# Optimization experiments

Measured on AMD Instinct MI355X. Metric: run time of the kernel, lower is better.

Reference implementation:

```python
import jax, jax.numpy as jnp
import numpy as np

EPS = 1e-6

def _ln(x, g, b):
    m = jnp.mean(x, -1, keepdims=True)
    v = jnp.mean((x - m) ** 2, -1, keepdims=True)
    return (x - m) * jax.lax.rsqrt(v + 1e-5) * g + b

def _mha(qin, kin, vin, wq, bq, wk, bk, wv, bv, wo, bo, nh=8):
    B, T, D = qin.shape
    S = kin.shape[1]
    dh = D // nh
    q = (qin @ wq + bq).reshape(B, T, nh, dh)
    k = (kin @ wk + bk).reshape(B, S, nh, dh)
    v = (vin @ wv + bv).reshape(B, S, nh, dh)
    a = jax.nn.softmax(jnp.einsum('bthd,bshd->bhts', q, k) / np.float32(np.sqrt(dh)), -1)
    o = jnp.einsum('bhts,bshd->bthd', a, v).reshape(B, T, D)
    return o @ wo + bo

def _sinu_pe(pos, num_feats=128, temperature=20.0):
    # pos: [..., 2] (x, y); returns [..., 2*num_feats] ordered (y-feats, x-feats)
    dim_t = temperature ** ((2 * (jnp.arange(num_feats) // 2)) / num_feats)
    e = pos[..., None] * (2 * np.pi) / dim_t  # [..., 2, F]
    e = jnp.stack([jnp.sin(e[..., 0::2]), jnp.cos(e[..., 1::2])], -1).reshape(e.shape)
    return jnp.concatenate([e[..., 1, :], e[..., 0, :]], -1)

def _spatial36(b1, b2, sizes):
    # b1, b2: [B, Q, 4]; sizes: [B, 2] = (h, w). UPT-style 18 feats + log -> 36.
    h = sizes[:, 0:1]; w = sizes[:, 1:2]
    c1x = (b1[..., 0] + b1[..., 2]) / 2; c1y = (b1[..., 1] + b1[..., 3]) / 2
    c2x = (b2[..., 0] + b2[..., 2]) / 2; c2y = (b2[..., 1] + b2[..., 3]) / 2
    w1 = b1[..., 2] - b1[..., 0]; h1 = b1[..., 3] - b1[..., 1]
    w2 = b2[..., 2] - b2[..., 0]; h2 = b2[..., 3] - b2[..., 1]
    a1 = w1 * h1; a2 = w2 * h2
    dx = jnp.abs(c2x - c1x) / (w1 + EPS)
    dy = jnp.abs(c2y - c1y) / (h1 + EPS)
    ix = jnp.clip(jnp.minimum(b1[..., 2], b2[..., 2]) - jnp.maximum(b1[..., 0], b2[..., 0]), 0)
    iy = jnp.clip(jnp.minimum(b1[..., 3], b2[..., 3]) - jnp.maximum(b1[..., 1], b2[..., 1]), 0)
    inter = ix * iy
    iou = inter / (a1 + a2 - inter + EPS)
    f = jnp.stack([c1x / w, c1y / h, c2x / w, c2y / h, w1 / w, h1 / h, w2 / w, h2 / h,
                   a1 / (h * w), a2 / (h * w), a2 / (a1 + EPS), w1 / (h1 + EPS), w2 / (h2 + EPS), iou,
                   (c2x > c1x) * dx, (c2x < c1x) * dx, (c2y > c1y) * dy, (c2y < c1y) * dy], -1)
    return jnp.concatenate([f, jnp.log(f + EPS)], -1)

def _forward(boxes, embeds, image_sizes, pose, line, sw1, sb1, sw2, sb2, sw3, sb3, bw, bb, pw, pb, lw, lb, enc_pe_w, enc_pe_b, enc_qkv_w, enc_qkv_b, enc_out_w, enc_out_b, enc_ff1_w, enc_ff1_b, enc_ff2_w, enc_ff2_b, enc_ln1_g, enc_ln1_b, enc_ln2_g, enc_ln2_b, dec_q_w, dec_q_b, dec_kv_w, dec_kv_b, dec_out_w, dec_out_b, dec_ff1_w, dec_ff1_b, dec_ff2_w, dec_ff2_b, dec_ln1_g, dec_ln1_b, dec_ln2_g, dec_ln2_b, fc1_w, fc1_b, fc2_w, fc2_b, mln1_g, mln1_b, mln2_g, mln2_b, m1_w, m1_b, m2_w, m2_b, labels, nh):
    B, N, _ = boxes.shape
    # static human-object pairing (x != y) & (x < nh)
    xg, yg = np.meshgrid(np.arange(N), np.arange(N), indexing='ij')
    keep = (xg != yg) & (xg < nh)
    xk = jnp.asarray(xg[keep]); yk = jnp.asarray(yg[keep])  # [P]
    # line features: adaptive-avg-pool(1,1) + 1x1 conv == spatial mean + linear
    line_feat = jnp.mean(line, axis=(2, 3)) @ lw + lb  # [B, 256]
    # spatial head on all N*N ordered pairs, then gather kept pairs
    xa = jnp.asarray(xg.reshape(-1)); ya = jnp.asarray(yg.reshape(-1))
    f36 = _spatial36(boxes[:, xa], boxes[:, ya], image_sizes)  # [B, N*N, 36]
    s = jax.nn.relu(f36 @ sw1 + sb1)
    s = jax.nn.relu(s @ sw2 + sb2)
    s = jax.nn.relu(s @ sw3 + sb3)
    spa = s.reshape(B, N, N, -1)[:, xk, yk]  # [B, P, R]
    # box sinusoidal positional encodings (cat of centre-PE and wh-PE)
    whwh = image_sizes[:, jnp.array([1, 0, 1, 0])][:, None]  # [B,1,4]
    bxn = boxes / whwh
    ctr = (bxn[..., :2] + bxn[..., 2:]) / 2
    whb = bxn[..., 2:] - bxn[..., :2]
    box_pe = jnp.concatenate([_sinu_pe(ctr), _sinu_pe(whb)], -1)  # [B, N, 512]
    # 2-layer transformer encoder over instance tokens (pos added to q,k)
    posx = box_pe @ enc_pe_w + enc_pe_b
    x = embeds
    for i in range(enc_qkv_w.shape[0]):
        wq, wk_, wv = jnp.split(enc_qkv_w[i], 3, axis=1)
        bq, bk_, bv = jnp.split(enc_qkv_b[i], 3)
        qk = x + posx
        att = _mha(qk, qk, x, wq, bq, wk_, bk_, wv, bv, enc_out_w[i], enc_out_b[i])
        x = _ln(x + att, enc_ln1_g[i], enc_ln1_b[i])
        ff = jax.nn.relu(x @ enc_ff1_w[i] + enc_ff1_b[i]) @ enc_ff2_w[i] + enc_ff2_b[i]
        x = _ln(x + ff, enc_ln2_g[i], enc_ln2_b[i])
    # pair gather + human/object positional embeds (box PE projected + line feature)
    pe_h = box_pe[:, xk] @ bw + bb + line_feat[:, None, :]
    pe_o = box_pe[:, yk] @ bw + bb + line_feat[:, None, :]
    h = x[:, xk]; o = x[:, yk]  # [B, P, 256]
    pose_ctx = pose @ pw + pb  # [B, M, 256]
    # HO refine decoder: cross-attention from pair tokens to pose tokens
    for l in range(dec_q_w.shape[0]):
        wk_, wv = jnp.split(dec_kv_w[l], 2, axis=1)
        bk_, bv = jnp.split(dec_kv_b[l], 2)
        def _layer(feat, pe):
            att = _mha(feat + pe, pose_ctx, pose_ctx, dec_q_w[l], dec_q_b[l], wk_, bk_, wv, bv, dec_out_w[l], dec_out_b[l])
            feat = _ln(feat + att, dec_ln1_g[l], dec_ln1_b[l])
            ff = jax.nn.relu(feat @ dec_ff1_w[l] + dec_ff1_b[l]) @ dec_ff2_w[l] + dec_ff2_b[l]
            return _ln(feat + ff, dec_ln2_g[l], dec_ln2_b[l])
        h = _layer(h, pe_h)
        o = _layer(o, pe_o)
    # multi-modal fusion
    ho = jnp.concatenate([h, o], -1)  # [B, P, 512]
    ho = _ln(ho @ fc1_w + fc1_b, mln1_g, mln1_b)
    sp = _ln(spa @ fc2_w + fc2_b, mln2_g, mln2_b)
    z = jax.nn.relu(jnp.concatenate([ho, sp], -1))
    z = jax.nn.relu(z @ m1_w + m1_b)
    z = jax.nn.relu(z @ m2_w + m2_b)
    return z  # [B, P, 256] HOI query features

def setup_inputs() -> dict:
    key = jax.random.key(0)
    ks = iter(jax.random.split(key, 80))
    B, N, NH, M, HH, WW = 16, 128, 32, 64, 8, 8
    W = 0.05
    def rn(shape, s=1.0):
        return jax.random.normal(next(ks), shape, dtype=jnp.float32) * s
    def ru(shape):
        return jax.random.uniform(next(ks), shape, dtype=jnp.float32)
    sizes = 800.0 + 480.0 * ru((B, 2))  # (h, w)
    wh = sizes[:, jnp.array([1, 0])]
    xy = ru((B, N, 2)) * wh[:, None] * 0.7
    bwh = ru((B, N, 2)) * wh[:, None] * 0.25 + 4.0
    boxes = jnp.concatenate([xy, xy + bwh], -1)
    labels = jnp.concatenate([jnp.zeros((B, NH), jnp.int32), jax.random.randint(next(ks), (B, N - NH), 1, 81, dtype=jnp.int32)], -1)
    return dict(
        boxes=boxes, embeds=rn((B, N, 256)), image_sizes=sizes, pose=rn((B, M, 768)), line=rn((B, 2048, HH, WW)),
        sw1=rn((36, 128), W), sb1=jnp.zeros((128,)), sw2=rn((128, 256), W), sb2=jnp.zeros((256,)), sw3=rn((256, 256), W), sb3=jnp.zeros((256,)),
        bw=rn((512, 256), W), bb=jnp.zeros((256,)), pw=rn((768, 256), W), pb=jnp.zeros((256,)), lw=rn((2048, 256), W), lb=jnp.zeros((256,)),
        enc_pe_w=rn((512, 256), W), enc_pe_b=jnp.zeros((256,)),
        enc_qkv_w=rn((2, 256, 768), W), enc_qkv_b=jnp.zeros((2, 768)), enc_out_w=rn((2, 256, 256), W), enc_out_b=jnp.zeros((2, 256)),
        enc_ff1_w=rn((2, 256, 1024), W), enc_ff1_b=jnp.zeros((2, 1024)), enc_ff2_w=rn((2, 1024, 256), W), enc_ff2_b=jnp.zeros((2, 256)),
        enc_ln1_g=jnp.ones((2, 256)), enc_ln1_b=jnp.zeros((2, 256)), enc_ln2_g=jnp.ones((2, 256)), enc_ln2_b=jnp.zeros((2, 256)),
        dec_q_w=rn((2, 256, 256), W), dec_q_b=jnp.zeros((2, 256)), dec_kv_w=rn((2, 256, 512), W), dec_kv_b=jnp.zeros((2, 512)),
        dec_out_w=rn((2, 256, 256), W), dec_out_b=jnp.zeros((2, 256)),
        dec_ff1_w=rn((2, 256, 1024), W), dec_ff1_b=jnp.zeros((2, 1024)), dec_ff2_w=rn((2, 1024, 256), W), dec_ff2_b=jnp.zeros((2, 256)),
        dec_ln1_g=jnp.ones((2, 256)), dec_ln1_b=jnp.zeros((2, 256)), dec_ln2_g=jnp.ones((2, 256)), dec_ln2_b=jnp.zeros((2, 256)),
        fc1_w=rn((512, 256), W), fc1_b=jnp.zeros((256,)), fc2_w=rn((256, 256), W), fc2_b=jnp.zeros((256,)),
        mln1_g=jnp.ones((256,)), mln1_b=jnp.zeros((256,)), mln2_g=jnp.ones((256,)), mln2_b=jnp.zeros((256,)),
        m1_w=rn((512, 384), W), m1_b=jnp.zeros((384,)), m2_w=rn((384, 256), W), m2_b=jnp.zeros((256,)),
        labels=labels, nh=NH)

def reference(boxes, embeds, image_sizes, pose, line, sw1, sb1, sw2, sb2, sw3, sb3, bw, bb, pw, pb, lw, lb, enc_pe_w, enc_pe_b, enc_qkv_w, enc_qkv_b, enc_out_w, enc_out_b, enc_ff1_w, enc_ff1_b, enc_ff2_w, enc_ff2_b, enc_ln1_g, enc_ln1_b, enc_ln2_g, enc_ln2_b, dec_q_w, dec_q_b, dec_kv_w, dec_kv_b, dec_out_w, dec_out_b, dec_ff1_w, dec_ff1_b, dec_ff2_w, dec_ff2_b, dec_ln1_g, dec_ln1_b, dec_ln2_g, dec_ln2_b, fc1_w, fc1_b, fc2_w, fc2_b, mln1_g, mln1_b, mln2_g, mln2_b, m1_w, m1_b, m2_w, m2_b, labels, nh):
    return _forward(boxes, embeds, image_sizes, pose, line, sw1, sb1, sw2, sb2, sw3, sb3, bw, bb, pw, pb, lw, lb, enc_pe_w, enc_pe_b, enc_qkv_w, enc_qkv_b, enc_out_w, enc_out_b, enc_ff1_w, enc_ff1_b, enc_ff2_w, enc_ff2_b, enc_ln1_g, enc_ln1_b, enc_ln2_g, enc_ln2_b, dec_q_w, dec_q_b, dec_kv_w, dec_kv_b, dec_out_w, dec_out_b, dec_ff1_w, dec_ff1_b, dec_ff2_w, dec_ff2_b, dec_ln1_g, dec_ln1_b, dec_ln2_g, dec_ln2_b, fc1_w, fc1_b, fc2_w, fc2_b, mln1_g, mln1_b, mln2_g, mln2_b, m1_w, m1_b, m2_w, m2_b, labels, nh)
```

## Files before the change

### kernel.cpp

```cpp
#include <hip/hip_runtime.h>
#include <stdint.h>

static constexpr int B      = 16;
static constexpr int N      = 128;
static constexpr int P      = 4064;
static constexpr int MPOSE  = 64;
static constexpr int64_t BN = (int64_t)B * N;
static constexpr int64_t BP = (int64_t)B * P;

#define TWO_PI 6.283185307179586f
#define QSCALE 0.17677669529663687f

typedef __attribute__((ext_vector_type(4))) float f32x4;
typedef __attribute__((ext_vector_type(8))) short bf16x8;
typedef __attribute__((ext_vector_type(8))) unsigned short u16x8;
typedef __attribute__((ext_vector_type(4))) unsigned short u16x4;

__device__ __forceinline__ unsigned short f2bf(float f) {
    union { float f; unsigned u; } v; v.f = f;
    unsigned r = (v.u + 0x7fffu + ((v.u >> 16) & 1u)) >> 16;
    return (unsigned short)r;
}
__device__ __forceinline__ float bf2f(unsigned short u) {
    union { unsigned u; float f; } v; v.u = (unsigned)u << 16;
    return v.f;
}
__device__ __forceinline__ void pair_xy(int p, int& x, int& y) {
    x = p / 127;
    int r = p - x * 127;
    y = (r < x) ? r : r + 1;
}
__device__ __forceinline__ int xcd_swz(int orig, int nwg) {
    int q = nwg >> 3, r = nwg & 7;
    int xcd = orig & 7, idx = orig >> 3;
    return (xcd < r ? xcd * (q + 1) : r * (q + 1) + (xcd - r) * q) + idx;
}
__device__ __forceinline__ void gld16(const unsigned short* g, unsigned short* l) {
    __builtin_amdgcn_global_load_lds(
        (const __attribute__((address_space(1))) void*)g,
        (__attribute__((address_space(3))) void*)l, 16, 0, 0);
}

struct WDesc { const float* src; int64_t dstOff; int K, Nn, Kpad, blockStart; };
struct WTable { WDesc d[29]; int nDesc; };

__global__ __launch_bounds__(256) void wprep_all_k(WTable t, unsigned short* __restrict__ wt)
{
    __shared__ float s[32][33];
    int bid = blockIdx.x;
    int di = 0;
    for (int i = 1; i < t.nDesc; ++i) if (t.d[i].blockStart <= bid) di = i;
    const WDesc& d = t.d[di];
    int lbid = bid - d.blockStart;
    int kTiles = d.Kpad >> 5;
    int k0 = (lbid % kTiles) * 32, n0 = (lbid / kTiles) * 32;
    int tx = threadIdx.x & 31, ty = threadIdx.x >> 5;
#pragma unroll
    for (int i = 0; i < 4; ++i) {
        int k = k0 + ty + i * 8;
        s[ty + i * 8][tx] = (k < d.K) ? d.src[(int64_t)k * d.Nn + n0 + tx] : 0.f;
    }
    __syncthreads();
    unsigned short* dst = wt + d.dstOff;
#pragma unroll
    for (int i = 0; i < 4; ++i) {
        int n = n0 + ty + i * 8;
        dst[(int64_t)n * d.Kpad + k0 + tx] = f2bf(s[tx][ty + i * 8]);
    }
}

template <bool RELU_OUT>
__global__ __launch_bounds__(256) void bgemm_k(
    const float* __restrict__ A, const float* __restrict__ A2, int lda,
    const unsigned short* __restrict__ Bt, int ldk,
    const float* __restrict__ bias,
    const float* __restrict__ Cadd, int addLd,
    const float* __restrict__ lfp,
    float* __restrict__ C, int ldc,
    int kSteps)
{
    __shared__ unsigned short As[128][40];
    __shared__ unsigned short Bs[128][40];
    const int tid  = threadIdx.x;
    const int lane = tid & 63;
    const int wave = tid >> 6;
    const int wr = wave >> 1, wc = wave & 1;
    const int row0 = blockIdx.y * 128, col0 = blockIdx.x * 128;
    const int l15 = lane & 15, l4 = lane >> 4;
    const int sr = tid >> 1;
    const int sh = (tid & 1) * 16;

    f32x4 acc[4][4] = {};

    for (int ks = 0; ks < kSteps; ++ks) {
        const int k0 = ks * 32;
        {
            const int64_t off = (int64_t)(row0 + sr) * lda + k0 + sh;
            const float* ap = A + off;
            float v[16];
#pragma unroll
            for (int i = 0; i < 4; ++i) {
                float4 tv = ((const float4*)ap)[i];
                v[i*4+0] = tv.x; v[i*4+1] = tv.y; v[i*4+2] = tv.z; v[i*4+3] = tv.w;
            }
            if (A2) {
                const float* ap2 = A2 + off;
#pragma unroll
                for (int i = 0; i < 4; ++i) {
                    float4 tv = ((const float4*)ap2)[i];
                    v[i*4+0] += tv.x; v[i*4+1] += tv.y; v[i*4+2] += tv.z; v[i*4+3] += tv.w;
                }
            }
            u16x8 p0, p1;
#pragma unroll
            for (int j = 0; j < 8; ++j) { p0[j] = f2bf(v[j]); p1[j] = f2bf(v[8 + j]); }
            *(u16x8*)&As[sr][sh]     = p0;
            *(u16x8*)&As[sr][sh + 8] = p1;
        }
        {
            const unsigned short* bp = Bt + (int64_t)(col0 + sr) * ldk + k0 + sh;
            *(u16x8*)&Bs[sr][sh]     = *(const u16x8*)bp;
            *(u16x8*)&Bs[sr][sh + 8] = *(const u16x8*)(bp + 8);
        }
        __syncthreads();
        bf16x8 af[4], bfr[4];
#pragma unroll
        for (int f = 0; f < 4; ++f) {
            af[f]  = *(const bf16x8*)&As[wr * 64 + f * 16 + l15][l4 * 8];
            bfr[f] = *(const bf16x8*)&Bs[wc * 64 + f * 16 + l15][l4 * 8];
        }
#pragma unroll
        for (int i = 0; i < 4; ++i)
#pragma unroll
            for (int j = 0; j < 4; ++j)
                acc[i][j] = __builtin_amdgcn_mfma_f32_16x16x32_bf16(af[i], bfr[j], acc[i][j], 0, 0, 0);
        __syncthreads();
    }
#pragma unroll
    for (int i = 0; i < 4; ++i) {
        int rb = row0 + wr * 64 + i * 16 + l4 * 4;
#pragma unroll
        for (int j = 0; j < 4; ++j) {
            int c = col0 + wc * 64 + j * 16 + l15;
            float bv = bias ? bias[c] : 0.f;
#pragma unroll
            for (int e = 0; e < 4; ++e) {
                int r = rb + e;
                float vv = acc[i][j][e] + bv;
                if (Cadd && c < addLd) vv += Cadd[(int64_t)r * addLd + c];
                if (lfp) vv += lfp[(r >> 7) * 256 + c];
                if (RELU_OUT) vv = fmaxf(vv, 0.f);
                C[(int64_t)r * ldc + c] = vv;
            }
        }
    }
}

static void bgemm(hipStream_t st,
                  const float* A, const float* A2, int lda,
                  const unsigned short* Bt, int ldk, const float* bias,
                  const float* Cadd, int addLd, const float* lfp,
                  float* C, int ldc, int M, int Ncols, int K, bool reluOut)
{
    dim3 g(Ncols / 128, M / 128), b(256);
    if (reluOut) bgemm_k<true><<<g,b,0,st>>>(A,A2,lda,Bt,ldk,bias,Cadd,addLd,lfp,C,ldc,K/32);
    else         bgemm_k<false><<<g,b,0,st>>>(A,A2,lda,Bt,ldk,bias,Cadd,addLd,lfp,C,ldc,K/32);
}

__global__ __launch_bounds__(256) void tgemm_k(
    const float* __restrict__ A, int lda,
    const unsigned short* __restrict__ Bt, int ldk,
    const float* __restrict__ bias,
    const float* __restrict__ res,
    const float* __restrict__ g, const float* __restrict__ be,
    float* __restrict__ C, int kSteps)
{
    __shared__ unsigned short As[64][40];
    __shared__ unsigned short Bs[256][40];
    __shared__ float partS[64][4], partQ[64][4];
    __shared__ float statM[64], statI[64];
    const int tid = threadIdx.x;
    const int lane = tid & 63, w = tid >> 6;
    const int l15 = lane & 15, l4 = lane >> 4;
    const int row0 = blockIdx.x * 64;
    const int sra = tid >> 2, sha = (tid & 3) * 8;

    f32x4 acc[4][4] = {};
    for (int ks = 0; ks < kSteps; ++ks) {
        int k0 = ks * 32;
        {
            const float* ap = A + (int64_t)(row0 + sra) * lda + k0 + sha;
            float4 t0 = ((const float4*)ap)[0];
            float4 t1 = ((const float4*)ap)[1];
            u16x8 p;
            p[0]=f2bf(t0.x); p[1]=f2bf(t0.y); p[2]=f2bf(t0.z); p[3]=f2bf(t0.w);
            p[4]=f2bf(t1.x); p[5]=f2bf(t1.y); p[6]=f2bf(t1.z); p[7]=f2bf(t1.w);
            *(u16x8*)&As[sra][sha] = p;
        }
        {
            const unsigned short* bp = Bt + (int64_t)tid * ldk + k0;
#pragma unroll
            for (int q = 0; q < 4; ++q)
                *(u16x8*)&Bs[tid][q * 8] = *(const u16x8*)(bp + q * 8);
        }
        __syncthreads();
        bf16x8 af[4], bfr[4];
#pragma unroll
        for (int f = 0; f < 4; ++f) {
            af[f]  = *(const bf16x8*)&As[f * 16 + l15][l4 * 8];
            bfr[f] = *(const bf16x8*)&Bs[w * 64 + f * 16 + l15][l4 * 8];
        }
#pragma unroll
        for (int i = 0; i < 4; ++i)
#pragma unroll
            for (int j = 0; j < 4; ++j)
                acc[i][j] = __builtin_amdgcn_mfma_f32_16x16x32_bf16(af[i], bfr[j], acc[i][j], 0, 0, 0);
        __syncthreads();
    }
    float ps[4][4] = {}, pq[4][4] = {};
#pragma unroll
    for (int i = 0; i < 4; ++i)
#pragma unroll
    for (int j = 0; j < 4; ++j) {
        int c = w * 64 + j * 16 + l15;
#pragma unroll
        for (int e = 0; e < 4; ++e) {
            int r = i * 16 + l4 * 4 + e;
            float v = acc[i][j][e] + bias[c] + res[(int64_t)(row0 + r) * 256 + c];
            acc[i][j][e] = v;
            ps[i][e] += v;
            pq[i][e] += v * v;
        }
    }
#pragma unroll
    for (int i = 0; i < 4; ++i)
#pragma unroll
    for (int e = 0; e < 4; ++e) {
#pragma unroll
        for (int m = 1; m < 16; m <<= 1) {
            ps[i][e] += __shfl_xor(ps[i][e], m);
            pq[i][e] += __shfl_xor(pq[i][e], m);
        }
    }
    if (l15 == 0) {
#pragma unroll
        for (int i = 0; i < 4; ++i)
#pragma unroll
        for (int e = 0; e < 4; ++e) {
            int r = i * 16 + l4 * 4 + e;
            partS[r][w] = ps[i][e];
            partQ[r][w] = pq[i][e];
        }
    }
    __syncthreads();
    if (tid < 64) {
        float s = partS[tid][0] + partS[tid][1] + partS[tid][2] + partS[tid][3];
        float q = partQ[tid][0] + partQ[tid][1] + partQ[tid][2] + partQ[tid][3];
        float m = s * (1.f/256.f);
        float var = q * (1.f/256.f) - m * m;
        statM[tid] = m;
        statI[tid] = rsqrtf(var + 1e-5f);
    }
    __syncthreads();
#pragma unroll
    for (int i = 0; i < 4; ++i)
#pragma unroll
    for (int j = 0; j < 4; ++j) {
        int c = w * 64 + j * 16 + l15;
#pragma unroll
        for (int e = 0; e < 4; ++e) {
            int r = i * 16 + l4 * 4 + e;
            C[(int64_t)(row0 + r) * 256 + c] = (acc[i][j][e] - statM[r]) * statI[r] * g[c] + be[c];
        }
    }
}

template <bool RELU_OUT, bool OUT_BF16>
__global__ __launch_bounds__(256) void hgemm_k(
    const unsigned short* __restrict__ A, int lda,
    const unsigned short* __restrict__ Bt, int ldk,
    const float* __restrict__ bias,
    void* __restrict__ Cv, int ldc,
    int kSteps, int nx)
{
    __shared__ unsigned short As[128][32];
    __shared__ unsigned short Bs[128][32];
    const int tid  = threadIdx.x;
    const int lane = tid & 63;
    const int wave = tid >> 6;
    const int wr = wave >> 1, wc = wave & 1;
    const int wgid = xcd_swz(blockIdx.x, gridDim.x);
    const int row0 = (wgid / nx) * 128, col0 = (wgid % nx) * 128;
    const int l15 = lane & 15, l4 = lane >> 4;
    const int srow = lane >> 2;
    const int scol = (lane & 3) * 8;

    f32x4 acc[4][4] = {};

    for (int ks = 0; ks < kSteps; ++ks) {
        const int k0 = ks * 32;
#pragma unroll
        for (int i = 0; i < 2; ++i) {
            int seg = wave * 2 + i;
            int r = seg * 16 + srow;
            gld16(A  + (int64_t)(row0 + r) * lda + k0 + scol, &As[seg * 16][0]);
            gld16(Bt + (int64_t)(col0 + r) * ldk + k0 + scol, &Bs[seg * 16][0]);
        }
        __syncthreads();
        bf16x8 af[4], bfr[4];
#pragma unroll
        for (int f = 0; f < 4; ++f) {
            af[f]  = *(const bf16x8*)&As[wr * 64 + f * 16 + l15][l4 * 8];
            bfr[f] = *(const bf16x8*)&Bs[wc * 64 + f * 16 + l15][l4 * 8];
        }
#pragma unroll
        for (int i = 0; i < 4; ++i)
#pragma unroll
            for (int j = 0; j < 4; ++j)
                acc[i][j] = __builtin_amdgcn_mfma_f32_16x16x32_bf16(af[i], bfr[j], acc[i][j], 0, 0, 0);
        __syncthreads();
    }
#pragma unroll
    for (int i = 0; i < 4; ++i) {
        int rb = row0 + wr * 64 + i * 16 + l4 * 4;
#pragma unroll
        for (int j = 0; j < 4; ++j) {
            int c = col0 + wc * 64 + j * 16 + l15;
            float bv = bias ? bias[c] : 0.f;
#pragma unroll
            for (int e = 0; e < 4; ++e) {
                int64_t off = (int64_t)(rb + e) * ldc + c;
                float vv = acc[i][j][e] + bv;
                if (RELU_OUT) vv = fmaxf(vv, 0.f);
                if (OUT_BF16) ((unsigned short*)Cv)[off] = f2bf(vv);
                else          ((float*)Cv)[off] = vv;
            }
        }
    }
}

__global__ __launch_bounds__(256) void spa_k(
    const float* __restrict__ boxes, const float* __restrict__ sizes,
    const unsigned short* __restrict__ W1, const float* __restrict__ b1,
    const unsigned short* __restrict__ W2, const float* __restrict__ b2,
    unsigned short* __restrict__ t3out, int chunk0)
{
    __shared__ unsigned short F[128][72];
    __shared__ unsigned short Bs[128][40];
    __shared__ unsigned short D1s[128][136];
    const int tid  = threadIdx.x;
    const int lane = tid & 63;
    const int wave = tid >> 6;
    const int wr = wave >> 1, wc = wave & 1;
    const int row0 = blockIdx.x * 128;
    const int l15 = lane & 15, l4 = lane >> 4;
    const int sr = tid >> 1;
    const int sh = (tid & 1) * 16;

    if (tid < 128) {
        int gp = chunk0 + row0 + tid;
        int b = gp / P, p = gp - b * P;
        int xi, yi; pair_xy(p, xi, yi);
        const float* b1x = boxes + ((int64_t)b * N + xi) * 4;
        const float* b2x = boxes + ((int64_t)b * N + yi) * 4;
        float h = sizes[b * 2 + 0], w = sizes[b * 2 + 1];
        float c1x = (b1x[0] + b1x[2]) * 0.5f, c1y = (b1x[1] + b1x[3]) * 0.5f;
        float c2x = (b2x[0] + b2x[2]) * 0.5f, c2y = (b2x[1] + b2x[3]) * 0.5f;
        float w1 = b1x[2] - b1x[0], h1 = b1x[3] - b1x[1];
        float w2 = b2x[2] - b2x[0], h2 = b2x[3] - b2x[1];
        float a1 = w1 * h1, a2 = w2 * h2;
        float dx = fabsf(c2x - c1x) / (w1 + 1e-6f);
        float dy = fabsf(c2y - c1y) / (h1 + 1e-6f);
        float ix = fmaxf(fminf(b1x[2], b2x[2]) - fmaxf(b1x[0], b2x[0]), 0.f);
        float iy = fmaxf(fminf(b1x[3], b2x[3]) - fmaxf(b1x[1], b2x[1]), 0.f);
        float inter = ix * iy;
        float iou = inter / (a1 + a2 - inter + 1e-6f);
        float f[18];
        f[0] = c1x / w;  f[1] = c1y / h;  f[2] = c2x / w;  f[3] = c2y / h;
        f[4] = w1 / w;   f[5] = h1 / h;   f[6] = w2 / w;   f[7] = h2 / h;
        f[8] = a1 / (h * w); f[9] = a2 / (h * w); f[10] = a2 / (a1 + 1e-6f);
        f[11] = w1 / (h1 + 1e-6f); f[12] = w2 / (h2 + 1e-6f); f[13] = iou;
        f[14] = (c2x > c1x) ? dx : 0.f;  f[15] = (c2x < c1x) ? dx : 0.f;
        f[16] = (c2y > c1y) ? dy : 0.f;  f[17] = (c2y < c1y) ? dy : 0.f;
#pragma unroll
        for (int i = 0; i < 18; ++i) {
            F[tid][i]      = f2bf(f[i]);
            F[tid][18 + i] = f2bf(logf(f[i] + 1e-6f));
        }
#pragma unroll
        for (int i = 36; i < 64; ++i) F[tid][i] = 0;
    }
    __syncthreads();

    f32x4 acc1[4][4] = {};
    for (int ks = 0; ks < 2; ++ks) {
        const int k0 = ks * 32;
        {
            const unsigned short* bp = W1 + (int64_t)sr * 64 + k0 + sh;
            *(u16x8*)&Bs[sr][sh]     = *(const u16x8*)bp;
            *(u16x8*)&Bs[sr][sh + 8] = *(const u16x8*)(bp + 8);
        }
        __syncthreads();
        bf16x8 af[4], bfr[4];
#pragma unroll
        for (int f = 0; f < 4; ++f) {
            af[f]  = *(const bf16x8*)&F[wr * 64 + f * 16 + l15][k0 + l4 * 8];
            bfr[f] = *(const bf16x8*)&Bs[wc * 64 + f * 16 + l15][l4 * 8];
        }
#pragma unroll
        for (int i = 0; i < 4; ++i)
#pragma unroll
            for (int j = 0; j < 4; ++j)
                acc1[i][j] = __builtin_amdgcn_mfma_f32_16x16x32_bf16(af[i], bfr[j], acc1[i][j], 0, 0, 0);
        __syncthreads();
    }
#pragma unroll
    for (int i = 0; i < 4; ++i) {
        int rb = wr * 64 + i * 16 + l4 * 4;
#pragma unroll
        for (int j = 0; j < 4; ++j) {
            int c = wc * 64 + j * 16 + l15;
            float bv = b1[c];
#pragma unroll
            for (int e = 0; e < 4; ++e)
                D1s[rb + e][c] = f2bf(fmaxf(acc1[i][j][e] + bv, 0.f));
        }
    }
    __syncthreads();

    f32x4 acc2[2][4][4] = {};
#pragma unroll
    for (int n = 0; n < 2; ++n) {
        for (int kk = 0; kk < 4; ++kk) {
            {
                const unsigned short* bp = W2 + (int64_t)(n * 128 + sr) * 128 + kk * 32 + sh;
                *(u16x8*)&Bs[sr][sh]     = *(const u16x8*)bp;
                *(u16x8*)&Bs[sr][sh + 8] = *(const u16x8*)(bp + 8);
            }
            __syncthreads();
            bf16x8 af[4], bfr[4];
#pragma unroll
            for (int f = 0; f < 4; ++f) {
                af[f]  = *(const bf16x8*)&D1s[wr * 64 + f * 16 + l15][kk * 32 + l4 * 8];
                bfr[f] = *(const bf16x8*)&Bs[wc * 64 + f * 16 + l15][l4 * 8];
            }
#pragma unroll
            for (int i = 0; i < 4; ++i)
#pragma unroll
                for (int j = 0; j < 4; ++j)
                    acc2[n][i][j] = __builtin_amdgcn_mfma_f32_16x16x32_bf16(af[i], bfr[j], acc2[n][i][j], 0, 0, 0);
            __syncthreads();
// ... 29 lines not shown
    int b = gp / P, p = gp - b * P;
    int xi, yi; pair_xy(p, xi, yi);
    int c = lane * 4;
    {
        float4 u  = *(const float4*)(UV + ((int64_t)(b * 128 + xi)) * 512 + c);
        float4 vv = *(const float4*)(UV + ((int64_t)(b * 128 + yi)) * 512 + 256 + c);
        float4 fbv = *(const float4*)(fb + c);
        float4 v;
        v.x = u.x + vv.x + fbv.x; v.y = u.y + vv.y + fbv.y;
        v.z = u.z + vv.z + fbv.z; v.w = u.w + vv.w + fbv.w;
        float s  = v.x + v.y + v.z + v.w;
        float sq = v.x*v.x + v.y*v.y + v.z*v.z + v.w*v.w;
#pragma unroll
        for (int off = 1; off < 64; off <<= 1) {
            s  += __shfl_xor(s, off);
            sq += __shfl_xor(sq, off);
        }
        float m = s * (1.f/256.f);
        float var = sq * (1.f/256.f) - m * m;
        float inv = rsqrtf(var + 1e-5f);
        float4 gg = *(const float4*)(g1 + c);
        float4 bb = *(const float4*)(be1 + c);
        u16x4 o;
        o[0] = f2bf(fmaxf((v.x - m) * inv * gg.x + bb.x, 0.f));
        o[1] = f2bf(fmaxf((v.y - m) * inv * gg.y + bb.y, 0.f));
        o[2] = f2bf(fmaxf((v.z - m) * inv * gg.z + bb.z, 0.f));
        o[3] = f2bf(fmaxf((v.w - m) * inv * gg.w + bb.w, 0.f));
        *(u16x4*)(zb + (int64_t)li * 512 + c) = o;
    }
    {
        u16x4 u = *(const u16x4*)(t3 + (int64_t)li * 256 + c);
        float4 v;
        v.x = bf2f(u[0]); v.y = bf2f(u[1]); v.z = bf2f(u[2]); v.w = bf2f(u[3]);
        float s  = v.x + v.y + v.z + v.w;
        float sq = v.x*v.x + v.y*v.y + v.z*v.z + v.w*v.w;
#pragma unroll
        for (int off = 1; off < 64; off <<= 1) {
            s  += __shfl_xor(s, off);
            sq += __shfl_xor(sq, off);
        }
        float m = s * (1.f/256.f);
        float var = sq * (1.f/256.f) - m * m;
        float inv = rsqrtf(var + 1e-5f);
        float4 gg = *(const float4*)(g2 + c);
        float4 bb = *(const float4*)(be2 + c);
        u16x4 o;
        o[0] = f2bf(fmaxf((v.x - m) * inv * gg.x + bb.x, 0.f));
        o[1] = f2bf(fmaxf((v.y - m) * inv * gg.y + bb.y, 0.f));
        o[2] = f2bf(fmaxf((v.z - m) * inv * gg.z + bb.z, 0.f));
        o[3] = f2bf(fmaxf((v.w - m) * inv * gg.w + bb.w, 0.f));
        *(u16x4*)(zb + (int64_t)li * 512 + 256 + c) = o;
    }
}

__global__ __launch_bounds__(256) void line_mean_k(const float* __restrict__ line, float* __restrict__ lm)
{
    int wave = threadIdx.x >> 6, lane = threadIdx.x & 63;
    int bc = blockIdx.x * 4 + wave;
    float v = line[(int64_t)bc * 64 + lane];
#pragma unroll
    for (int off = 1; off < 64; off <<= 1) v += __shfl_xor(v, off);
    if (lane == 0) lm[bc] = v * (1.f/64.f);
}

__global__ __launch_bounds__(256) void line_proj_k(
    const float* __restrict__ lm, const float* __restrict__ lw,
    const float* __restrict__ lb, float* __restrict__ lf)
{
    __shared__ float red[8][32];
    int b = blockIdx.y, jg = blockIdx.x;
    int jj = threadIdx.x & 31, cc = threadIdx.x >> 5;
    int j = jg * 32 + jj;
    const float* lmb = lm + (int64_t)b * 2048 + cc * 256;
    const float* lwp = lw + (int64_t)(cc * 256) * 256 + j;
    float acc = 0.f;
#pragma unroll 4
    for (int k = 0; k < 256; ++k) acc += lmb[k] * lwp[(int64_t)k * 256];
    red[cc][jj] = acc;
    __syncthreads();
    if (cc == 0) {
        float s = lb[j];
#pragma unroll
        for (int i = 0; i < 8; ++i) s += red[i][jj];
        lf[b * 256 + j] = s;
    }
}

__global__ __launch_bounds__(512) void boxpe_k(
    const float* __restrict__ boxes, const float* __restrict__ sizes, float* __restrict__ boxpe)
{
    int row = blockIdx.x;
    int b = row >> 7;
    int i = threadIdx.x;
    const float* bx = boxes + (int64_t)row * 4;
    float h = sizes[b * 2 + 0], w = sizes[b * 2 + 1];
    float x0 = bx[0] / w, y0 = bx[1] / h, x1 = bx[2] / w, y1 = bx[3] / h;
    int seg = i >> 7, j = i & 127, k = j >> 1;
    float val;
    switch (seg) {
        case 0: val = (y0 + y1) * 0.5f; break;
        case 1: val = (x0 + x1) * 0.5f; break;
        case 2: val = (y1 - y0); break;
        default: val = (x1 - x0); break;
    }
    float dimt = exp2f((float)k * (4.321928094887362f / 64.f));
    float arg = val * TWO_PI / dimt;
    boxpe[(int64_t)row * 512 + i] = (j & 1) ? cosf(arg) : sinf(arg);
}

__global__ __launch_bounds__(128) void enc_attn_k(
    const float* __restrict__ qkv, float* __restrict__ outp)
{
    int b = blockIdx.x >> 3, hd = blockIdx.x & 7;
    __shared__ float kl[128][32];
    __shared__ float vl[128][32];
    int tid = threadIdx.x;
    for (int i = tid; i < 128 * 32; i += 128) {
        int s = i >> 5, j = i & 31;
        const float* rp = qkv + ((int64_t)(b * 128 + s)) * 768 + hd * 32 + j;
        kl[s][j] = rp[256];
        vl[s][j] = rp[512];
    }
    __syncthreads();
    int t = tid;
    const float* qp = qkv + ((int64_t)(b * 128 + t)) * 768 + hd * 32;
    float qr[32];
#pragma unroll
    for (int j = 0; j < 32; ++j) qr[j] = qp[j] * QSCALE;
    float m = -1e30f, l = 0.f;
    for (int s = 0; s < 128; ++s) {
        float d = 0.f;
#pragma unroll
        for (int j = 0; j < 32; ++j) d += qr[j] * kl[s][j];
        float mn = fmaxf(m, d);
        l = l * __expf(m - mn) + __expf(d - mn);
        m = mn;
    }
    float acc[32] = {};
    for (int s = 0; s < 128; ++s) {
        float d = 0.f;
#pragma unroll
        for (int j = 0; j < 32; ++j) d += qr[j] * kl[s][j];
        float wgt = __expf(d - m);
#pragma unroll
        for (int j = 0; j < 32; ++j) acc[j] += wgt * vl[s][j];
    }
    float linv = 1.f / l;
    float* op = outp + ((int64_t)(b * 128 + t)) * 256 + hd * 32;
#pragma unroll
    for (int j = 0; j < 32; ++j) op[j] = acc[j] * linv;
}

__global__ __launch_bounds__(256) void dec_attn_k(
    const float* __restrict__ q, const float* __restrict__ kv,
    float* __restrict__ outp, int rows, int rpb)
{
    int hd = blockIdx.y;
    int r0 = blockIdx.x * 256;
    __shared__ float kl[2][64][32];
    __shared__ float vl[2][64][32];
    int tid = threadIdx.x;
    int b0 = r0 / rpb;
    int b1 = (r0 + 255) / rpb;
    if (b1 >= B) b1 = B - 1;
    for (int i = tid; i < 64 * 32; i += 256) {
        int s = i >> 5, j = i & 31;
        int64_t off0 = ((int64_t)(b0 * MPOSE + s)) * 512 + hd * 32 + j;
        int64_t off1 = ((int64_t)(b1 * MPOSE + s)) * 512 + hd * 32 + j;
        kl[0][s][j] = kv[off0];
        vl[0][s][j] = kv[off0 + 256];
        kl[1][s][j] = kv[off1];
        vl[1][s][j] = kv[off1 + 256];
    }
    __syncthreads();
    int r = r0 + tid;
    if (r >= rows) return;
    int which = (r / rpb == b0) ? 0 : 1;
    int64_t qoff = (int64_t)r * 256 + hd * 32;
    float qr[32];
#pragma unroll
    for (int j = 0; j < 32; ++j) qr[j] = q[qoff + j] * QSCALE;
    float m = -1e30f, l = 0.f;
    for (int s = 0; s < 64; ++s) {
        float d = 0.f;
#pragma unroll
        for (int j = 0; j < 32; ++j) d += qr[j] * kl[which][s][j];
        float mn = fmaxf(m, d);
        l = l * __expf(m - mn) + __expf(d - mn);
        m = mn;
    }
    float acc[32] = {};
    for (int s = 0; s < 64; ++s) {
        float d = 0.f;
#pragma unroll
        for (int j = 0; j < 32; ++j) d += qr[j] * kl[which][s][j];
        float wgt = __expf(d - m);
#pragma unroll
        for (int j = 0; j < 32; ++j) acc[j] += wgt * vl[which][s][j];
    }
    float linv = 1.f / l;
#pragma unroll
    for (int j = 0; j < 32; ++j) outp[qoff + j] = acc[j] * linv;
}

static constexpr int64_t WT_QKV  = 0;
static constexpr int64_t WT_EOUT = WT_QKV  + 2*196608;
static constexpr int64_t WT_EFF1 = WT_EOUT + 2*65536;
static constexpr int64_t WT_EFF2 = WT_EFF1 + 2*262144;
static constexpr int64_t WT_DQ   = WT_EFF2 + 2*262144;
static constexpr int64_t WT_DKV  = WT_DQ   + 2*65536;
static constexpr int64_t WT_DOUT = WT_DKV  + 2*131072;
static constexpr int64_t WT_DFF1 = WT_DOUT + 2*65536;
static constexpr int64_t WT_DFF2 = WT_DFF1 + 2*262144;
static constexpr int64_t WT_SW1  = WT_DFF2 + 2*262144;
static constexpr int64_t WT_SW2  = WT_SW1 + 8192;
static constexpr int64_t WT_SW3  = WT_SW2 + 32768;
static constexpr int64_t WT_BW   = WT_SW3 + 65536;
static constexpr int64_t WT_PW   = WT_BW  + 131072;
static constexpr int64_t WT_EPE  = WT_PW  + 196608;
static constexpr int64_t WT_FC1  = WT_EPE + 131072;
static constexpr int64_t WT_FC2  = WT_FC1 + 131072;
static constexpr int64_t WT_M1   = WT_FC2 + 65536;
static constexpr int64_t WT_M2   = WT_M1  + 196608;
static constexpr int64_t WT_TOTAL = WT_M2 + 98304;

extern "C" void kernel_launch(void* const* d_in, const int* in_sizes, int n_in,
                              void* d_out, int out_size, void* d_ws, size_t ws_size,
                              hipStream_t stream)
{
    (void)in_sizes; (void)n_in; (void)out_size;
    const float* boxes     = (const float*)d_in[0];
    const float* embeds    = (const float*)d_in[1];
    const float* sizes     = (const float*)d_in[2];
    const float* pose      = (const float*)d_in[3];
    const float* line      = (const float*)d_in[4];
    const float* sw1 = (const float*)d_in[5];  const float* sb1 = (const float*)d_in[6];
    const float* sw2 = (const float*)d_in[7];  const float* sb2 = (const float*)d_in[8];
    const float* sw3 = (const float*)d_in[9];  const float* sb3 = (const float*)d_in[10];
    const float* bw  = (const float*)d_in[11]; const float* bb  = (const float*)d_in[12];
    const float* pw  = (const float*)d_in[13]; const float* pb  = (const float*)d_in[14];
    const float* lw  = (const float*)d_in[15]; const float* lb  = (const float*)d_in[16];
    const float* enc_pe_w  = (const float*)d_in[17]; const float* enc_pe_b = (const float*)d_in[18];
    const float* enc_qkv_w = (const float*)d_in[19]; const float* enc_qkv_b = (const float*)d_in[20];
    const float* enc_out_w = (const float*)d_in[21]; const float* enc_out_b = (const float*)d_in[22];
    const float* enc_ff1_w = (const float*)d_in[23]; const float* enc_ff1_b = (const float*)d_in[24];
    const float* enc_ff2_w = (const float*)d_in[25]; const float* enc_ff2_b = (const float*)d_in[26];
    const float* enc_ln1_g = (const float*)d_in[27]; const float* enc_ln1_b = (const float*)d_in[28];
    const float* enc_ln2_g = (const float*)d_in[29]; const float* enc_ln2_b = (const float*)d_in[30];
    const float* dec_q_w   = (const float*)d_in[31]; const float* dec_q_b  = (const float*)d_in[32];
    const float* dec_kv_w  = (const float*)d_in[33]; const float* dec_kv_b = (const float*)d_in[34];
    const float* dec_out_w = (const float*)d_in[35]; const float* dec_out_b = (const float*)d_in[36];
    const float* dec_ff1_w = (const float*)d_in[37]; const float* dec_ff1_b = (const float*)d_in[38];
    const float* dec_ff2_w = (const float*)d_in[39]; const float* dec_ff2_b = (const float*)d_in[40];
    const float* dec_ln1_g = (const float*)d_in[41]; const float* dec_ln1_b = (const float*)d_in[42];
    const float* dec_ln2_g = (const float*)d_in[43]; const float* dec_ln2_b = (const float*)d_in[44];
    const float* fc1_w = (const float*)d_in[45]; const float* fc1_b = (const float*)d_in[46];
    const float* fc2_w = (const float*)d_in[47]; const float* fc2_b = (const float*)d_in[48];
    const float* mln1_g = (const float*)d_in[49]; const float* mln1_b = (const float*)d_in[50];
    const float* mln2_g = (const float*)d_in[51]; const float* mln2_b = (const float*)d_in[52];
    const float* m1_w = (const float*)d_in[53]; const float* m1_b = (const float*)d_in[54];
    const float* m2_w = (const float*)d_in[55]; const float* m2_b = (const float*)d_in[56];
    float* out = (float*)d_out;

    float* base = (float*)d_ws;
    int64_t wsf = (int64_t)(ws_size / sizeof(float));
    float* x_   = base;
    float* bpw_ = x_   + 524288;
    float* lf   = bpw_ + 524288;
    float* kv0  = lf   + 4096;
    unsigned short* wt = (unsigned short*)(kv0 + 2 * 524288);
    float* arena = (float*)(wt + WT_TOTAL);
    const int64_t LIVE_F = arena - base;
    int64_t arena_f = wsf - LIVE_F;
    if (arena_f < 0) arena_f = 0;

    float* posx  = arena;
    float* boxpe = posx  + 524288;
    float* pqk0  = boxpe + 1048576;
    float* pqk1  = pqk0  + 1048576;
    float* e_qkv = pqk1  + 1048576;
    float* e_t   = e_qkv + 1572864;
    float* e_ff  = e_t   + 524288;
    float* pctx  = e_ff  + 2097152;
    float* lm    = pctx  + 262144;

    int64_t rc = ((arena_f * 2) / 1152) & ~127LL;
    if (rc > BP) rc = BP;
    if (rc < 128) rc = 128;

    {
        WTable T;
        int nd = 0, bs = 0;
        auto add = [&](const float* src, int64_t dstOff, int K, int Nn, int Kpad) {
            T.d[nd] = { src, dstOff, K, Nn, Kpad, bs };
            bs += (Kpad / 32) * (Nn / 32);
            ++nd;
        };
        for (int i = 0; i < 2; ++i) {
            add(enc_qkv_w + (int64_t)i*196608, WT_QKV  + i*196608, 256, 768, 256);
            add(enc_out_w + (int64_t)i*65536,  WT_EOUT + i*65536,  256, 256, 256);
            add(enc_ff1_w + (int64_t)i*262144, WT_EFF1 + i*262144, 256, 1024, 256);
            add(enc_ff2_w + (int64_t)i*262144, WT_EFF2 + i*262144, 1024, 256, 1024);
            add(dec_q_w   + (int64_t)i*65536,  WT_DQ   + i*65536,  256, 256, 256);
            add(dec_kv_w  + (int64_t)i*131072, WT_DKV  + i*131072, 256, 512, 256);
            add(dec_out_w + (int64_t)i*65536,  WT_DOUT + i*65536,  256, 256, 256);
            add(dec_ff1_w + (int64_t)i*262144, WT_DFF1 + i*262144, 256, 1024, 256);
            add(dec_ff2_w + (int64_t)i*262144, WT_DFF2 + i*262144, 1024, 256, 1024);
        }
        add(sw1, WT_SW1, 36, 128, 64);
        add(sw2, WT_SW2, 128, 256, 128);
        add(sw3, WT_SW3, 256, 256, 256);
        add(bw,  WT_BW,  512, 256, 512);
        add(pw,  WT_PW,  768, 256, 768);
        add(enc_pe_w, WT_EPE, 512, 256, 512);
        add(fc1_w,             WT_FC1,         256, 256, 256);
        add(fc1_w + 256 * 256, WT_FC1 + 65536, 256, 256, 256);
        add(fc2_w, WT_FC2, 256, 256, 256);
        add(m1_w, WT_M1, 512, 384, 512);
        add(m2_w, WT_M2, 384, 256, 384);
        T.nDesc = nd;
        wprep_all_k<<<bs, 256, 0, stream>>>(T, wt);
    }

    line_mean_k<<<8192, 256, 0, stream>>>(line, lm);
    line_proj_k<<<dim3(8, B), 256, 0, stream>>>(lm, lw, lb, lf);
    boxpe_k<<<(int)BN, 512, 0, stream>>>(boxes, sizes, boxpe);
    bgemm(stream, boxpe, nullptr, 512, wt + WT_EPE, 512, enc_pe_b, nullptr, 0, nullptr, posx, 256, (int)BN, 256, 512, false);
    bgemm(stream, boxpe, nullptr, 512, wt + WT_BW,  512, bb,       nullptr, 0, lf,      bpw_, 256, (int)BN, 256, 512, false);
    bgemm(stream, pose,  nullptr, 768, wt + WT_PW,  768, pb,       nullptr, 0, nullptr, pctx, 256, B*MPOSE, 256, 768, false);
    for (int l = 0; l < 2; ++l)
        bgemm(stream, pctx, nullptr, 256, wt + WT_DKV + l*131072, 256, dec_kv_b + (int64_t)l*512,
              nullptr, 0, nullptr, kv0 + (int64_t)l*524288, 512, B*MPOSE, 512, 256, false);
    bgemm(stream, posx, nullptr, 256, wt + WT_QKV,          256, nullptr, nullptr, 0, nullptr, pqk0, 512, (int)BN, 512, 256, false);
    bgemm(stream, posx, nullptr, 256, wt + WT_QKV + 196608, 256, nullptr, nullptr, 0, nullptr, pqk1, 512, (int)BN, 512, 256, false);

    for (int i = 0; i < 2; ++i) {
        const float* xin = (i == 0) ? embeds : x_;
        const float* pqk = (i == 0) ? pqk0 : pqk1;
        const unsigned short* Wq = wt + WT_QKV + (int64_t)i * 196608;
        bgemm(stream, xin, nullptr, 256, Wq, 256, enc_qkv_b + (int64_t)i*768, pqk, 512, nullptr,
              e_qkv, 768, (int)BN, 768, 256, false);
        enc_attn_k<<<B * 8, 128, 0, stream>>>(e_qkv, e_t);
        tgemm_k<<<(int)(BN / 64), 256, 0, stream>>>(e_t, 256, wt + WT_EOUT + (int64_t)i*65536, 256,
            enc_out_b + i*256, xin, enc_ln1_g + i*256, enc_ln1_b + i*256, x_, 8);
        bgemm(stream, x_, nullptr, 256, wt + WT_EFF1 + (int64_t)i*262144, 256, enc_ff1_b + i*1024,
              nullptr, 0, nullptr, e_ff, 1024, (int)BN, 1024, 256, true);
        tgemm_k<<<(int)(BN / 64), 256, 0, stream>>>(e_ff, 1024, wt + WT_EFF2 + (int64_t)i*262144, 1024,
            enc_ff2_b + i*256, x_, enc_ln2_g + i*256, enc_ln2_b + i*256, x_, 32);
    }

    for (int l = 0; l < 2; ++l) {
        bgemm(stream, x_, bpw_, 256, wt + WT_DQ + (int64_t)l*65536, 256, dec_q_b + l*256,
              nullptr, 0, nullptr, e_t, 256, (int)BN, 256, 256, false);
        dec_attn_k<<<dim3((int)(BN / 256), 8), 256, 0, stream>>>(e_t, kv0 + (int64_t)l*524288, e_qkv, (int)BN, N);
        tgemm_k<<<(int)(BN / 64), 256, 0, stream>>>(e_qkv, 256, wt + WT_DOUT + (int64_t)l*65536, 256,
            dec_out_b + l*256, x_, dec_ln1_g + l*256, dec_ln1_b + l*256, x_, 8);
        bgemm(stream, x_, nullptr, 256, wt + WT_DFF1 + (int64_t)l*262144, 256, dec_ff1_b + l*1024,
              nullptr, 0, nullptr, e_ff, 1024, (int)BN, 1024, 256, true);
        tgemm_k<<<(int)(BN / 64), 256, 0, stream>>>(e_ff, 1024, wt + WT_DFF2 + (int64_t)l*262144, 1024,
            dec_ff2_b + l*256, x_, dec_ln2_g + l*256, dec_ln2_b + l*256, x_, 32);
    }
    float* UV = kv0;
    bgemm(stream, x_, nullptr, 256, wt + WT_FC1, 256, nullptr, nullptr, 0, nullptr, UV, 512, (int)BN, 512, 256, false);

    for (int64_t c0 = 0; c0 < BP; c0 += rc) {
        int rows = (int)((BP - c0 < rc) ? (BP - c0) : rc);
        unsigned short* t3 = (unsigned short*)arena;
        unsigned short* zb = t3 + (int64_t)rc * 256;
        unsigned short* z2 = zb + (int64_t)rc * 512;

        spa_k<<<rows / 128, 256, 0, stream>>>(boxes, sizes,
            wt + WT_SW1, sb1, wt + WT_SW2, sb2, t3, (int)c0);
        hgemm_k<true,true><<<2 * (rows / 128), 256, 0, stream>>>(
            t3, 256, wt + WT_SW3, 256, sb3, z2, 256, 8, 2);
        hgemm_k<false,true><<<2 * (rows / 128), 256, 0, stream>>>(
            z2, 256, wt + WT_FC2, 256, fc2_b, t3, 256, 8, 2);
        zprep_k<<<rows / 4, 256, 0, stream>>>(UV, fc1_b, t3, mln1_g, mln1_b, mln2_g, mln2_b,
                                              zb, (int)c0, rows);
        hgemm_k<true,true><<<3 * (rows / 128), 256, 0, stream>>>(
            zb, 512, wt + WT_M1, 512, m1_b, z2, 384, 16, 3);
        hgemm_k<true,false><<<2 * (rows / 128), 256, 0, stream>>>(
            z2, 384, wt + WT_M2, 384, m2_b, out + c0 * 256, 256, 12, 2);
    }
}
```

Baseline: 913.5 us.

## Shrink LayerNorm GEMM tiles to 16 rows and batch KV/pos-QKV projections

The fused GEMM+residual+LayerNorm kernel now handles 16 rows per block instead of 64, so it launches four times as many blocks (128 instead of 32 for 2048 rows) and fills more compute units. Each block still reloads the full 256-column weight tile, so weight traffic per row goes up. The two decoder KV projections and the two positional QK projections are each merged into one wider GEMM launch. Downstream kernels read from these merged buffers through new stride parameters.

```diff
diff --git a/kernel.cpp b/kernel.cpp
--- a/kernel.cpp
+++ b/kernel.cpp
@@ -74,7 +74,7 @@
     const float* __restrict__ A, const float* __restrict__ A2, int lda,
     const unsigned short* __restrict__ Bt, int ldk,
     const float* __restrict__ bias,
-    const float* __restrict__ Cadd, int addLd,
+    const float* __restrict__ Cadd, int addStride, int addCols,
     const float* __restrict__ lfp,
     float* __restrict__ C, int ldc,
     int kSteps)
@@ -147,7 +147,7 @@
             for (int e = 0; e < 4; ++e) {
                 int r = rb + e;
                 float vv = acc[i][j][e] + bv;
-                if (Cadd && c < addLd) vv += Cadd[(int64_t)r * addLd + c];
+                if (Cadd && c < addCols) vv += Cadd[(int64_t)r * addStride + c];
                 if (lfp) vv += lfp[(r >> 7) * 256 + c];
                 if (RELU_OUT) vv = fmaxf(vv, 0.f);
                 C[(int64_t)r * ldc + c] = vv;
@@ -159,15 +159,15 @@
 static void bgemm(hipStream_t st,
                   const float* A, const float* A2, int lda,
                   const unsigned short* Bt, int ldk, const float* bias,
-                  const float* Cadd, int addLd, const float* lfp,
+                  const float* Cadd, int addStride, int addCols, const float* lfp,
                   float* C, int ldc, int M, int Ncols, int K, bool reluOut)
 {
     dim3 g(Ncols / 128, M / 128), b(256);
-    if (reluOut) bgemm_k<true><<<g,b,0,st>>>(A,A2,lda,Bt,ldk,bias,Cadd,addLd,lfp,C,ldc,K/32);
-    else         bgemm_k<false><<<g,b,0,st>>>(A,A2,lda,Bt,ldk,bias,Cadd,addLd,lfp,C,ldc,K/32);
-}
-
-__global__ __launch_bounds__(256) void tgemm_k(
+    if (reluOut) bgemm_k<true><<<g,b,0,st>>>(A,A2,lda,Bt,ldk,bias,Cadd,addStride,addCols,lfp,C,ldc,K/32);
+    else         bgemm_k<false><<<g,b,0,st>>>(A,A2,lda,Bt,ldk,bias,Cadd,addStride,addCols,lfp,C,ldc,K/32);
+}
+
+__global__ __launch_bounds__(256) void tgemm16_k(
     const float* __restrict__ A, int lda,
     const unsigned short* __restrict__ Bt, int ldk,
     const float* __restrict__ bias,
@@ -175,27 +175,26 @@
     const float* __restrict__ g, const float* __restrict__ be,
     float* __restrict__ C, int kSteps)
 {
-    __shared__ unsigned short As[64][40];
+    __shared__ unsigned short As[16][40];
     __shared__ unsigned short Bs[256][40];
-    __shared__ float partS[64][4], partQ[64][4];
-    __shared__ float statM[64], statI[64];
+    __shared__ float partS[16][4], partQ[16][4];
+    __shared__ float statM[16], statI[16];
     const int tid = threadIdx.x;
     const int lane = tid & 63, w = tid >> 6;
     const int l15 = lane & 15, l4 = lane >> 4;
-    const int row0 = blockIdx.x * 64;
-    const int sra = tid >> 2, sha = (tid & 3) * 8;
-
-    f32x4 acc[4][4] = {};
+    const int row0 = blockIdx.x * 16;
+
+    f32x4 acc[4] = {};
     for (int ks = 0; ks < kSteps; ++ks) {
         int k0 = ks * 32;
-        {
-            const float* ap = A + (int64_t)(row0 + sra) * lda + k0 + sha;
+        if (tid < 64) {
+            const float* ap = A + (int64_t)(row0 + (tid >> 2)) * lda + k0 + (tid & 3) * 8;
             float4 t0 = ((const float4*)ap)[0];
             float4 t1 = ((const float4*)ap)[1];
             u16x8 p;
             p[0]=f2bf(t0.x); p[1]=f2bf(t0.y); p[2]=f2bf(t0.z); p[3]=f2bf(t0.w);
             p[4]=f2bf(t1.x); p[5]=f2bf(t1.y); p[6]=f2bf(t1.z); p[7]=f2bf(t1.w);
-            *(u16x8*)&As[sra][sha] = p;
+            *(u16x8*)&As[tid >> 2][(tid & 3) * 8] = p;
         }
         {
             const unsigned short* bp = Bt + (int64_t)tid * ldk + k0;
@@ -204,56 +203,47 @@
                 *(u16x8*)&Bs[tid][q * 8] = *(const u16x8*)(bp + q * 8);
         }
         __syncthreads();
-        bf16x8 af[4], bfr[4];
-#pragma unroll
-        for (int f = 0; f < 4; ++f) {
-            af[f]  = *(const bf16x8*)&As[f * 16 + l15][l4 * 8];
+        bf16x8 af = *(const bf16x8*)&As[l15][l4 * 8];
+        bf16x8 bfr[4];
+#pragma unroll
+        for (int f = 0; f < 4; ++f)
             bfr[f] = *(const bf16x8*)&Bs[w * 64 + f * 16 + l15][l4 * 8];
-        }
-#pragma unroll
-        for (int i = 0; i < 4; ++i)
-#pragma unroll
-            for (int j = 0; j < 4; ++j)
-                acc[i][j] = __builtin_amdgcn_mfma_f32_16x16x32_bf16(af[i], bfr[j], acc[i][j], 0, 0, 0);
+#pragma unroll
+        for (int j = 0; j < 4; ++j)
+            acc[j] = __builtin_amdgcn_mfma_f32_16x16x32_bf16(af, bfr[j], acc[j], 0, 0, 0);
         __syncthreads();
     }
-    float ps[4][4] = {}, pq[4][4] = {};
-#pragma unroll
-    for (int i = 0; i < 4; ++i)
+    float ps[4] = {}, pq[4] = {};
 #pragma unroll
     for (int j = 0; j < 4; ++j) {
         int c = w * 64 + j * 16 + l15;
 #pragma unroll
         for (int e = 0; e < 4; ++e) {
-            int r = i * 16 + l4 * 4 + e;
-            float v = acc[i][j][e] + bias[c] + res[(int64_t)(row0 + r) * 256 + c];
-            acc[i][j][e] = v;
-            ps[i][e] += v;
-            pq[i][e] += v * v;
-        }
-    }
-#pragma unroll
-    for (int i = 0; i < 4; ++i)
+            int r = l4 * 4 + e;
+            float v = acc[j][e] + bias[c] + res[(int64_t)(row0 + r) * 256 + c];
+            acc[j][e] = v;
+            ps[e] += v;
+            pq[e] += v * v;
+        }
+    }
 #pragma unroll
     for (int e = 0; e < 4; ++e) {
 #pragma unroll
         for (int m = 1; m < 16; m <<= 1) {
-            ps[i][e] += __shfl_xor(ps[i][e], m);
-            pq[i][e] += __shfl_xor(pq[i][e], m);
+            ps[e] += __shfl_xor(ps[e], m);
+            pq[e] += __shfl_xor(pq[e], m);
         }
     }
     if (l15 == 0) {
 #pragma unroll
-        for (int i = 0; i < 4; ++i)
-#pragma unroll
         for (int e = 0; e < 4; ++e) {
-            int r = i * 16 + l4 * 4 + e;
-            partS[r][w] = ps[i][e];
-            partQ[r][w] = pq[i][e];
+            int r = l4 * 4 + e;
+            partS[r][w] = ps[e];
+            partQ[r][w] = pq[e];
         }
     }
     __syncthreads();
-    if (tid < 64) {
+    if (tid < 16) {
         float s = partS[tid][0] + partS[tid][1] + partS[tid][2] + partS[tid][3];
         float q = partQ[tid][0] + partQ[tid][1] + partQ[tid][2] + partQ[tid][3];
         float m = s * (1.f/256.f);
@@ -263,14 +253,12 @@
     }
     __syncthreads();
 #pragma unroll
-    for (int i = 0; i < 4; ++i)
-#pragma unroll
     for (int j = 0; j < 4; ++j) {
         int c = w * 64 + j * 16 + l15;
 #pragma unroll
         for (int e = 0; e < 4; ++e) {
-            int r = i * 16 + l4 * 4 + e;
-            C[(int64_t)(row0 + r) * 256 + c] = (acc[i][j][e] - statM[r]) * statI[r] * g[c] + be[c];
+            int r = l4 * 4 + e;
+            C[(int64_t)(row0 + r) * 256 + c] = (acc[j][e] - statM[r]) * statI[r] * g[c] + be[c];
         }
     }
 }
@@ -296,7 +284,6 @@
     const int scol = (lane & 3) * 8;
 
     f32x4 acc[4][4] = {};
-
     for (int ks = 0; ks < kSteps; ++ks) {
         const int k0 = ks * 32;
 #pragma unroll
@@ -632,7 +619,7 @@
 }
 
 __global__ __launch_bounds__(256) void dec_attn_k(
-    const float* __restrict__ q, const float* __restrict__ kv,
+    const float* __restrict__ q, const float* __restrict__ kv, int ldkv,
     float* __restrict__ outp, int rows, int rpb)
 {
     int hd = blockIdx.y;
@@ -645,8 +632,8 @@
     if (b1 >= B) b1 = B - 1;
     for (int i = tid; i < 64 * 32; i += 256) {
         int s = i >> 5, j = i & 31;
-        int64_t off0 = ((int64_t)(b0 * MPOSE + s)) * 512 + hd * 32 + j;
-        int64_t off1 = ((int64_t)(b1 * MPOSE + s)) * 512 + hd * 32 + j;
+        int64_t off0 = ((int64_t)(b0 * MPOSE + s)) * ldkv + hd * 32 + j;
+        int64_t off1 = ((int64_t)(b1 * MPOSE + s)) * ldkv + hd * 32 + j;
         kl[0][s][j] = kv[off0];
         vl[0][s][j] = kv[off0 + 256];
         kl[1][s][j] = kv[off1];
@@ -748,7 +735,7 @@
     float* bpw_ = x_   + 524288;
     float* lf   = bpw_ + 524288;
     float* kv0  = lf   + 4096;
-    unsigned short* wt = (unsigned short*)(kv0 + 2 * 524288);
+    unsigned short* wt = (unsigned short*)(kv0 + 1048576);
     float* arena = (float*)(wt + WT_TOTAL);
     const int64_t LIVE_F = arena - base;
     int64_t arena_f = wsf - LIVE_F;
@@ -756,9 +743,8 @@
 
     float* posx  = arena;
     float* boxpe = posx  + 524288;
-    float* pqk0  = boxpe + 1048576;
-    float* pqk1  = pqk0  + 1048576;
-    float* e_qkv = pqk1  + 1048576;
+    float* pqkv  = boxpe + 1048576;
+    float* e_qkv = pqkv  + 3145728;
     float* e_t   = e_qkv + 1572864;
     float* e_ff  = e_t   + 524288;
     float* pctx  = e_ff  + 2097152;
@@ -805,43 +791,45 @@
     line_mean_k<<<8192, 256, 0, stream>>>(line, lm);
     line_proj_k<<<dim3(8, B), 256, 0, stream>>>(lm, lw, lb, lf);
     boxpe_k<<<(int)BN, 512, 0, stream>>>(boxes, sizes, boxpe);
-    bgemm(stream, boxpe, nullptr, 512, wt + WT_EPE, 512, enc_pe_b, nullptr, 0, nullptr, posx, 256, (int)BN, 256, 512, false);
-    bgemm(stream, boxpe, nullptr, 512, wt + WT_BW,  512, bb,       nullptr, 0, lf,      bpw_, 256, (int)BN, 256, 512, false);
-    bgemm(stream, pose,  nullptr, 768, wt + WT_PW,  768, pb,       nullptr, 0, nullptr, pctx, 256, B*MPOSE, 256, 768, false);
-    for (int l = 0; l < 2; ++l)
-        bgemm(stream, pctx, nullptr, 256, wt + WT_DKV + l*131072, 256, dec_kv_b + (int64_t)l*512,
-              nullptr, 0, nullptr, kv0 + (int64_t)l*524288, 512, B*MPOSE, 512, 256, false);
-    bgemm(stream, posx, nullptr, 256, wt + WT_QKV,          256, nullptr, nullptr, 0, nullptr, pqk0, 512, (int)BN, 512, 256, false);
-    bgemm(stream, posx, nullptr, 256, wt + WT_QKV + 196608, 256, nullptr, nullptr, 0, nullptr, pqk1, 512, (int)BN, 512, 256, false);
+    bgemm(stream, boxpe, nullptr, 512, wt + WT_EPE, 512, enc_pe_b, nullptr, 0, 0, nullptr,
+          posx, 256, (int)BN, 256, 512, false);
+    bgemm(stream, boxpe, nullptr, 512, wt + WT_BW,  512, bb, nullptr, 0, 0, lf,
+          bpw_, 256, (int)BN, 256, 512, false);
+    bgemm(stream, pose,  nullptr, 768, wt + WT_PW,  768, pb, nullptr, 0, 0, nullptr,
+          pctx, 256, B*MPOSE, 256, 768, false);
+    bgemm(stream, pctx, nullptr, 256, wt + WT_DKV, 256, dec_kv_b, nullptr, 0, 0, nullptr,
+          kv0, 1024, B*MPOSE, 1024, 256, false);
+    bgemm(stream, posx, nullptr, 256, wt + WT_QKV, 256, nullptr, nullptr, 0, 0, nullptr,
+          pqkv, 1536, (int)BN, 1536, 256, false);
 
     for (int i = 0; i < 2; ++i) {
         const float* xin = (i == 0) ? embeds : x_;
-        const float* pqk = (i == 0) ? pqk0 : pqk1;
         const unsigned short* Wq = wt + WT_QKV + (int64_t)i * 196608;
-        bgemm(stream, xin, nullptr, 256, Wq, 256, enc_qkv_b + (int64_t)i*768, pqk, 512, nullptr,
-              e_qkv, 768, (int)BN, 768, 256, false);
+        bgemm(stream, xin, nullptr, 256, Wq, 256, enc_qkv_b + (int64_t)i*768,
+              pqkv + i*768, 1536, 512, nullptr, e_qkv, 768, (int)BN, 768, 256, false);
         enc_attn_k<<<B * 8, 128, 0, stream>>>(e_qkv, e_t);
-        tgemm_k<<<(int)(BN / 64), 256, 0, stream>>>(e_t, 256, wt + WT_EOUT + (int64_t)i*65536, 256,
+        tgemm16_k<<<(int)(BN / 16), 256, 0, stream>>>(e_t, 256, wt + WT_EOUT + (int64_t)i*65536, 256,
             enc_out_b + i*256, xin, enc_ln1_g + i*256, enc_ln1_b + i*256, x_, 8);
         bgemm(stream, x_, nullptr, 256, wt + WT_EFF1 + (int64_t)i*262144, 256, enc_ff1_b + i*1024,
-              nullptr, 0, nullptr, e_ff, 1024, (int)BN, 1024, 256, true);
-        tgemm_k<<<(int)(BN / 64), 256, 0, stream>>>(e_ff, 1024, wt + WT_EFF2 + (int64_t)i*262144, 1024,
+              nullptr, 0, 0, nullptr, e_ff, 1024, (int)BN, 1024, 256, true);
+        tgemm16_k<<<(int)(BN / 16), 256, 0, stream>>>(e_ff, 1024, wt + WT_EFF2 + (int64_t)i*262144, 1024,
             enc_ff2_b + i*256, x_, enc_ln2_g + i*256, enc_ln2_b + i*256, x_, 32);
     }
 
     for (int l = 0; l < 2; ++l) {
         bgemm(stream, x_, bpw_, 256, wt + WT_DQ + (int64_t)l*65536, 256, dec_q_b + l*256,
-              nullptr, 0, nullptr, e_t, 256, (int)BN, 256, 256, false);
-        dec_attn_k<<<dim3((int)(BN / 256), 8), 256, 0, stream>>>(e_t, kv0 + (int64_t)l*524288, e_qkv, (int)BN, N);
-        tgemm_k<<<(int)(BN / 64), 256, 0, stream>>>(e_qkv, 256, wt + WT_DOUT + (int64_t)l*65536, 256,
+              nullptr, 0, 0, nullptr, e_t, 256, (int)BN, 256, 256, false);
+        dec_attn_k<<<dim3((int)(BN / 256), 8), 256, 0, stream>>>(e_t, kv0 + l*512, 1024, e_qkv, (int)BN, N);
+        tgemm16_k<<<(int)(BN / 16), 256, 0, stream>>>(e_qkv, 256, wt + WT_DOUT + (int64_t)l*65536, 256,
             dec_out_b + l*256, x_, dec_ln1_g + l*256, dec_ln1_b + l*256, x_, 8);
         bgemm(stream, x_, nullptr, 256, wt + WT_DFF1 + (int64_t)l*262144, 256, dec_ff1_b + l*1024,
-              nullptr, 0, nullptr, e_ff, 1024, (int)BN, 1024, 256, true);
-        tgemm_k<<<(int)(BN / 64), 256, 0, stream>>>(e_ff, 1024, wt + WT_DFF2 + (int64_t)l*262144, 1024,
+              nullptr, 0, 0, nullptr, e_ff, 1024, (int)BN, 1024, 256, true);
+        tgemm16_k<<<(int)(BN / 16), 256, 0, stream>>>(e_ff, 1024, wt + WT_DFF2 + (int64_t)l*262144, 1024,
             dec_ff2_b + l*256, x_, dec_ln2_g + l*256, dec_ln2_b + l*256, x_, 32);
     }
     float* UV = kv0;
-    bgemm(stream, x_, nullptr, 256, wt + WT_FC1, 256, nullptr, nullptr, 0, nullptr, UV, 512, (int)BN, 512, 256, false);
+    bgemm(stream, x_, nullptr, 256, wt + WT_FC1, 256, nullptr, nullptr, 0, 0, nullptr,
+          UV, 512, (int)BN, 512, 256, false);
 
     for (int64_t c0 = 0; c0 < BP; c0 += rc) {
         int rows = (int)((BP - c0 < rc) ? (BP - c0) : rc);
```

Result: faster. 814.0 us (-10.9%).
